# Kernel tuning notes

Hardware: AMD Instinct MI355X
Metric: run time of the kernel (lower is better)

## Reference

```python
import jax, jax.numpy as jnp
import numpy as np

B = 4096

def setup_inputs() -> dict:
    key = jax.random.key(0)
    k1, k2, k3, k4, k5 = jax.random.split(key, 5)
    x = jax.random.normal(k1, (B, 3, 32, 32), dtype=jnp.float32)
    conv_w = jax.random.normal(k2, (45, 1, 5, 5), dtype=jnp.float32) * 0.2   # grouped conv: 3 groups x 15 filters, 1 in-ch each
    conv_b = jax.random.normal(k3, (45,), dtype=jnp.float32) * 0.1
    tree_w = jax.random.normal(k4, (1, 16, 15, 3, 7, 7, 2, 2), dtype=jnp.float32) * 0.05
    tree_b = jax.random.normal(k5, (1, 16, 3, 7), dtype=jnp.float32) * 0.1
    return {"x": x, "conv_w": conv_w, "conv_b": conv_b, "tree_w": tree_w, "tree_b": tree_b}

def _forward(x, conv_w, conv_b, tree_w, tree_b):
    # grouped conv: (B,3,32,32) -> (B,45,28,28), groups=3 (channel order is group-major)
    y = jax.lax.conv_general_dilated(
        x, conv_w, window_strides=(1, 1), padding='VALID',
        dimension_numbers=('NCHW', 'OIHW', 'NCHW'), feature_group_count=3)
    y = jax.nn.sigmoid(y + conv_b[None, :, None, None])
    # max_pool2d(2): (B,45,28,28) -> (B,45,14,14)
    y = jax.lax.reduce_window(y, -jnp.inf, jax.lax.max,
                              window_dimensions=(1, 1, 2, 2),
                              window_strides=(1, 1, 2, 2), padding='VALID')
    b = y.shape[0]
    # unfold(2,2,stride=2) + reshape/transpose chain == rearrange to
    # (b, f=15, g=3, ph=7, pw=7, ki=2, kj=2); channels c = g*15 + f, H = 2*ph+ki, W = 2*pw+kj
    y = y.reshape(b, 3, 15, 7, 2, 7, 2)            # (b, g, f, ph, ki, pw, kj)
    y = y.transpose(0, 2, 1, 3, 5, 4, 6)           # (b, f, g, ph, pw, ki, kj)
    # TreeLayer: broadcast multiply with W[1,16,15,3,7,7,2,2], sum over dims (15,7,2,2)
    w = tree_w[0]                                   # (o=16, f, g, ph, pw, ki, kj)
    out = jnp.einsum('bfghwij,ofghwij->bogh', y, w)  # (b,16,3,7)
    out = jax.nn.sigmoid(out + tree_b)              # bias (1,16,3,7) broadcasts
    return out.reshape(b, -1)                       # (b, 336)

def reference(x, conv_w, conv_b, tree_w, tree_b):
    return _forward(x, conv_w, conv_b, tree_w, tree_b)
```

## Files before the change

kernel.cpp:

```cpp
#include <hip/hip_runtime.h>
#include <hip/hip_fp16.h>
#include <math.h>


#define NTW   (21 * 15 * 16 * 32)
#define TWBYTES (NTW * 2)
#define WFRAG_HALFS (3 * 2 * 64 * 8)
#define WFRAG_BYTES (WFRAG_HALFS * 2)
#define POOL_STRIDE 10240
#define POOL_BYTES (POOL_STRIDE * 2)

typedef __fp16 h2v __attribute__((ext_vector_type(2)));
typedef short short8v __attribute__((ext_vector_type(8)));
typedef float float4v __attribute__((ext_vector_type(4)));
union HU { unsigned u; h2v v; };
union FRAG { uint4 u; short8v s; };

#if defined(__has_builtin)
#if __has_builtin(__builtin_amdgcn_fdot2)
#define HAVE_FDOT2 1
#endif
#endif

__device__ __forceinline__ float sigmoidf_(float v) {
    return 1.0f / (1.0f + __expf(-v));
}
__device__ __forceinline__ h2v as_h2(unsigned x) { HU t; t.u = x; return t.v; }
__device__ __forceinline__ ushort f2bf(float v) {
    unsigned u = __float_as_uint(v);
    u += 0x7fffu + ((u >> 16) & 1u);
    return (ushort)(u >> 16);
}
__device__ __forceinline__ unsigned cvtpk_bf16(float a, float b) {
    unsigned r;
    asm volatile("v_cvt_pk_bf16_f32 %0, %1, %2" : "=v"(r) : "v"(a), "v"(b));
    return r;
}
__device__ __forceinline__ unsigned pkrtz(float a, float b) {
    HU t; t.v = __builtin_amdgcn_cvt_pkrtz(a, b); return t.u;
}

__global__ __launch_bounds__(256) void prep_all(
    const float* __restrict__ tw, const float* __restrict__ cw,
    __half* __restrict__ tw2, ushort* __restrict__ wfrag)
{
    int i = blockIdx.x * 256 + threadIdx.x;
    if (i < NTW) {
        const int e   = i & 31;
        const int o   = (i >> 5) & 15;
        const int fgh = i >> 9;
        const int f   = fgh % 15, gh = fgh / 15;
        const int g   = gh / 7,  h  = gh % 7;
        const int parity = e >> 4, rem = e & 15, half = rem >> 3, pxl = rem & 7;
        float v = 0.f;
        if (pxl < 7) {
            const int px = half * 7 + pxl;
            const int w = px >> 1, j = px & 1;
            v = tw[o * 8820 + f * 588 + g * 196 + h * 28 + w * 4 + parity * 2 + j];
        }
        tw2[i] = __float2half(v);
        return;
    }
    const int j5 = i - NTW;
    if (j5 >= 384) return;
    const int g  = j5 >> 7, rem = j5 & 127, fr = rem >> 6, l = rem & 63;
    const int f  = l & 15, q = l >> 4;
    ushort o[8];
    #pragma unroll
    for (int j = 0; j < 8; ++j) {
        float v = 0.f;
        if (f < 15 && j < 5) {
            if (fr == 0)           v = cw[(g * 15 + f) * 25 + q * 5 + j];
            else if (q == 0)       v = cw[(g * 15 + f) * 25 + 20 + j];
        }
        o[j] = f2bf(v);
    }
    ushort* d = wfrag + ((g * 2 + fr) * 64 + l) * 8;
    *(uint4*)d = make_uint4(
        (unsigned)o[0] | ((unsigned)o[1] << 16),
        (unsigned)o[2] | ((unsigned)o[3] << 16),
        (unsigned)o[4] | ((unsigned)o[5] << 16),
        (unsigned)o[6] | ((unsigned)o[7] << 16));
}

__global__ __launch_bounds__(256) void conv_pool_mfma(
    const float* __restrict__ x,
    const float* __restrict__ cb,
    const ushort* __restrict__ wfrag,
    __half* __restrict__ pool16,
    int B)
{
    __shared__ __align__(16) float  s_xf[32 * 40];
    __shared__ __align__(16) ushort s_W[32 * 30 * 8];
    __shared__ __align__(16) ushort s_pool[105 * 40];
    __shared__ float s_cb[45];
    __shared__ __align__(16) ushort s_zero[8];

    const int b = blockIdx.x;
    if (b >= B) return;
    const int t = threadIdx.x;
    const int lane = t & 63, wv = t >> 6;
    const int q = lane >> 4, oxl = lane & 15;

    if (t < 45) s_cb[t] = cb[t];
    if (t == 45) *(uint4*)&s_zero[0] = make_uint4(0u, 0u, 0u, 0u);

    float4 xpre[3];
    {
        const float4* x4 = (const float4*)(x + (size_t)b * 3072);
        #pragma unroll
        for (int g = 0; g < 3; ++g) xpre[g] = x4[g * 256 + t];
    }
    FRAG w1[3], w2[3];
    {
        const uint4* wf4 = (const uint4*)wfrag;
        #pragma unroll
        for (int g2 = 0; g2 < 3; ++g2) {
            w1[g2].u = wf4[(g2 * 2 + 0) * 64 + lane];
            w2[g2].u = wf4[(g2 * 2 + 1) * 64 + lane];
        }
    }

    const float4v z4 = {0.f, 0.f, 0.f, 0.f};
    const int row_s = t >> 3, q_s = t & 7;

    #pragma unroll 1
    for (int g = 0; g < 3; ++g) {
        *(float4*)&s_xf[row_s * 40 + q_s * 4] = xpre[g];
        if (t < 64) {
            const int r2 = t >> 1, k = t & 1;
            *(float4*)&s_xf[r2 * 40 + 32 + k * 4] = make_float4(0.f, 0.f, 0.f, 0.f);
        }
        __syncthreads();

        #pragma unroll 1
        for (int task = t; task < 480; task += 256) {
            const int row = task / 15, m = task % 15;
            const float* src = &s_xf[row * 40 + 2 * m];
            float f[10];
            #pragma unroll
            for (int k = 0; k < 5; ++k)
                *(float2*)&f[2 * k] = *(const float2*)&src[2 * k];
            const unsigned e0 = cvtpk_bf16(f[0], f[1]), e1 = cvtpk_bf16(f[2], f[3]);
            const unsigned e2 = cvtpk_bf16(f[4], f[5]), e3 = cvtpk_bf16(f[6], f[7]);
            const unsigned o0 = cvtpk_bf16(f[1], f[2]), o1 = cvtpk_bf16(f[3], f[4]);
            const unsigned o2 = cvtpk_bf16(f[5], f[6]), o3 = cvtpk_bf16(f[7], f[8]);
            ushort* wb = &s_W[(row * 30 + 2 * m) * 8];
            *(uint4*)wb       = make_uint4(e0, e1, e2, e3);
            *(uint4*)(wb + 8) = make_uint4(o0, o1, o2, o3);
        }
        __syncthreads();

        #pragma unroll 1
        for (int i = 0; i < 7; ++i) {
            const int p = wv * 7 + i;
            const int py = p >> 1, half = p & 1;
            const ushort* base = &s_W[(2 * py + q) * 240 + (oxl + 14 * half) * 8];

            FRAG a10, a11, a20, a21;
            a10.u = *(const uint4*)base;
            a11.u = *(const uint4*)(base + 240);
            const ushort* p20 = (q == 0)
                ? &s_W[(2 * py + 4) * 240 + oxl * 8 + half * 112] : &s_zero[0];
            const ushort* p21 = (q == 0)
                ? &s_W[(2 * py + 5) * 240 + oxl * 8 + half * 112] : &s_zero[0];
            a20.u = *(const uint4*)p20;
            a21.u = *(const uint4*)p21;

            float4v acc0 = __builtin_amdgcn_mfma_f32_16x16x32_bf16(a20.s, w2[g].s, z4, 0, 0, 0);
            acc0 = __builtin_amdgcn_mfma_f32_16x16x32_bf16(a10.s, w1[g].s, acc0, 0, 0, 0);
            float4v acc1 = __builtin_amdgcn_mfma_f32_16x16x32_bf16(a21.s, w2[g].s, z4, 0, 0, 0);
            acc1 = __builtin_amdgcn_mfma_f32_16x16x32_bf16(a11.s, w1[g].s, acc1, 0, 0, 0);

            const int f = oxl;
            if (f < 15) {
                const float bias = s_cb[g * 15 + f];
                const float p0 = fmaxf(fmaxf(acc0[0], acc0[1]), fmaxf(acc1[0], acc1[1]));
                const float p1 = fmaxf(fmaxf(acc0[2], acc0[3]), fmaxf(acc1[2], acc1[3]));
                const float s0 = sigmoidf_(p0 + bias);
                const float s1 = (q < 3) ? sigmoidf_(p1 + bias) : 0.f;
                const int chunk = f * 7 + (py >> 1);
                const int e0i = (py & 1) * 16 + half * 8 + 2 * q;
                *(unsigned*)&s_pool[chunk * 40 + e0i] = pkrtz(s0, s1);
            }
        }
        __syncthreads();

        {
            uint4* dst4 = (uint4*)(pool16 + (size_t)b * POOL_STRIDE) + g * 420;
            for (int i = t; i < 420; i += 256) {
                const int chunk = i >> 2, k = i & 3;
                dst4[i] = *(const uint4*)&s_pool[chunk * 40 + k * 8];
            }
        }
        __syncthreads();
    }
}

__global__ __launch_bounds__(256) void tree_kernel(
    const __half* __restrict__ pool16,
    const __half* __restrict__ tw2,
    const float* __restrict__ tb,
    float* __restrict__ out,
    int B, int nblk)
{
    __shared__ float s_red[256 * 17];

    const int cpx = nblk / 8;
    const int sid = (blockIdx.x % 8) * cpx + blockIdx.x / 8;
    const int gh = sid % 21, tile = sid / 21;
    const int g = gh / 7, h = gh % 7;

    const int t  = threadIdx.x;
    const int bl = t & 63, fg = t >> 6;
    const int b  = tile * 64 + bl;
    if (b >= B) return;

    const int f0 = fg * 4;
    const int nf = (fg < 3) ? 4 : 3;

    float acc[16];
    #pragma unroll
    for (int o = 0; o < 16; ++o) acc[o] = 0.f;

    #pragma unroll 1
    for (int fi = 0; fi < nf; ++fi) {
        const int f = f0 + fi;
        const uint4* pc = (const uint4*)(pool16 + (size_t)b * POOL_STRIDE
                                         + ((g * 15 + f) * 7 + h) * 32);
        const uint4* wc = (const uint4*)(tw2 + (size_t)((gh * 15 + f) * 16) * 32);
        uint4 pu[4];
        #pragma unroll
        for (int k = 0; k < 4; ++k) pu[k] = pc[k];
        #pragma unroll
        for (int o = 0; o < 16; ++o) {
            #pragma unroll
            for (int k = 0; k < 4; ++k) {
                const uint4 wu = wc[o * 4 + k];
#ifdef HAVE_FDOT2
                acc[o] = __builtin_amdgcn_fdot2(as_h2(pu[k].x), as_h2(wu.x), acc[o], false);
                acc[o] = __builtin_amdgcn_fdot2(as_h2(pu[k].y), as_h2(wu.y), acc[o], false);
                acc[o] = __builtin_amdgcn_fdot2(as_h2(pu[k].z), as_h2(wu.z), acc[o], false);
                acc[o] = __builtin_amdgcn_fdot2(as_h2(pu[k].w), as_h2(wu.w), acc[o], false);
#else
                const unsigned pw[4] = {pu[k].x, pu[k].y, pu[k].z, pu[k].w};
                const unsigned ww[4] = {wu.x, wu.y, wu.z, wu.w};
                #pragma unroll
                for (int qq = 0; qq < 4; ++qq) {
                    acc[o] += __half2float(__ushort_as_half((ushort)(pw[qq] & 0xffff)))
                            * __half2float(__ushort_as_half((ushort)(ww[qq] & 0xffff)));
                    acc[o] += __half2float(__ushort_as_half((ushort)(pw[qq] >> 16)))
                            * __half2float(__ushort_as_half((ushort)(ww[qq] >> 16)));
                }
#endif
            }
        }
    }

    #pragma unroll
    for (int o = 0; o < 16; ++o) s_red[t * 17 + o] = acc[o];
    __syncthreads();

    const int og = t >> 6;
    #pragma unroll
    for (int m = 0; m < 4; ++m) {
        const int o = og * 4 + m;
        float a = s_red[(0 * 64 + bl) * 17 + o] + s_red[(1 * 64 + bl) * 17 + o]
                + s_red[(2 * 64 + bl) * 17 + o] + s_red[(3 * 64 + bl) * 17 + o];
        const int idx = o * 21 + gh;
        out[(size_t)b * 336 + idx] = sigmoidf_(a + tb[idx]);
    }
}

__global__ __launch_bounds__(256) void tree_backbone_legacy(
    const float* __restrict__ x, const float* __restrict__ cw,
    const float* __restrict__ cb, const float* __restrict__ tw,
    const float* __restrict__ tb, float* __restrict__ out, int B)
{
    __shared__ float s_x[3 * 32 * 36];
    __shared__ float s_cwl[45 * 25];
    __shared__ float s_cb[45];
    __shared__ float s_pool[45][197];

    const int b = blockIdx.x;
    if (b >= B) return;
    const int t = threadIdx.x;

    const float4* xs = (const float4*)(x + (size_t)b * 3072);
    for (int i = t; i < 768; i += 256) {
        const float4 v = xs[i];
        const int g = i >> 8, rem = i & 255, r = rem >> 3, qq = rem & 7;
        const int p = ((r & 1) << 4) + (r >> 1);
        *(float4*)&s_x[(g * 32 + p) * 36 + qq * 4] = v;
    }
    for (int i = t; i < 1125; i += 256) s_cwl[i] = cw[i];
    if (t < 45) s_cb[t] = cb[t];
    __syncthreads();

    for (int task = t; task < 1260; task += 256) {
        const int h  = (task >= 630) ? 1 : 0;
        const int tt = task - 630 * h;
        const int c  = tt / 14;
        const int py = tt - c * 14;
        const int g  = c / 15;
        float aA[14], aB[14];
        #pragma unroll
        for (int d = 0; d < 14; ++d) { aA[d] = 0.f; aB[d] = 0.f; }
        #pragma unroll
        for (int dr = 0; dr < 6; ++dr) {
            const float* rp = s_x + (g * 32 + ((dr & 1) << 4) + py + (dr >> 1)) * 36 + 12 * h;
            float f[20];
            #pragma unroll
            for (int k = 0; k < 5; ++k)
                *(float4*)&f[4 * k] = *(const float4*)&rp[4 * k];
            if (dr <= 4)
                #pragma unroll
                for (int kx = 0; kx < 5; ++kx) {
                    const float w = s_cwl[c * 25 + dr * 5 + kx];
                    #pragma unroll
                    for (int d = 0; d < 14; ++d) aA[d] += f[d + kx + 2 * h] * w;
                }
            if (dr >= 1)
                #pragma unroll
                for (int kx = 0; kx < 5; ++kx) {
                    const float w = s_cwl[c * 25 + (dr - 1) * 5 + kx];
                    #pragma unroll
                    for (int d = 0; d < 14; ++d) aB[d] += f[d + kx + 2 * h] * w;
                }
        }
        float* dst = &s_pool[c][py * 14 + 7 * h];
        #pragma unroll
        for (int p = 0; p < 7; ++p) {
            float m = fmaxf(fmaxf(aA[2 * p], aA[2 * p + 1]),
                            fmaxf(aB[2 * p], aB[2 * p + 1]));
            dst[p] = sigmoidf_(m + s_cb[c]);
        }
    }
    __syncthreads();

    for (int idx = t; idx < 336; idx += 256) {
        const int o  = idx / 21;
        const int r2 = idx - o * 21;
        const int g  = r2 / 7;
        const int hh = r2 - g * 7;
        const float* wp = tw + o * 8820 + g * 196 + hh * 28;
        float acc = 0.0f;
        #pragma unroll 1
        for (int f = 0; f < 15; ++f) {
            const float4* wf = (const float4*)(wp + f * 588);
            const float* p0 = &s_pool[g * 15 + f][(2 * hh) * 14];
            const float* p1 = p0 + 14;
            #pragma unroll
            for (int w = 0; w < 7; ++w) {
                const float4 qv = wf[w];
                acc += p0[2 * w] * qv.x + p0[2 * w + 1] * qv.y
                     + p1[2 * w] * qv.z + p1[2 * w + 1] * qv.w;
            }
        }
        out[(size_t)b * 336 + idx] = sigmoidf_(acc + tb[idx]);
    }
}

extern "C" void kernel_launch(void* const* d_in, const int* in_sizes, int n_in,
                              void* d_out, int out_size, void* d_ws, size_t ws_size,
                              hipStream_t stream) {
    const float* x  = (const float*)d_in[0];
    const float* cw = (const float*)d_in[1];
    const float* cb = (const float*)d_in[2];
    const float* tw = (const float*)d_in[3];
    const float* tb = (const float*)d_in[4];
    float* out = (float*)d_out;

    const int B = in_sizes[0] / 3072;
    const size_t need = (size_t)TWBYTES + (size_t)WFRAG_BYTES + (size_t)B * POOL_BYTES;
    if (ws_size >= need) {
        __half* tw2    = (__half*)d_ws;
        ushort* wfrag  = (ushort*)((char*)d_ws + TWBYTES);
        __half* pool16 = (__half*)((char*)d_ws + TWBYTES + WFRAG_BYTES);
        const int nblk = (B / 64) * 21;
        prep_all<<<(NTW + 384 + 255) / 256, 256, 0, stream>>>(tw, cw, tw2, wfrag);
        conv_pool_mfma<<<B, 256, 0, stream>>>(x, cb, wfrag, pool16, B);
        tree_kernel<<<nblk, 256, 0, stream>>>(pool16, tw2, tb, out, B, nblk);
    } else {
        tree_backbone_legacy<<<B, 256, 0, stream>>>(x, cw, cb, tw, tb, out, B);
    }
}
```

Before: 136.3 us.

## Fuse tree layer into conv-pool kernel, keeping pooled activations in LDS

Merges the conv/pool kernel and the tree kernel into one per-sample kernel. The pooled fp16 activations for all three groups now stay in shared memory instead of going through a global buffer of about 20 KB per sample. Tree weights are re-laid out so each thread owns one (channel, row) chunk and reads coalesced weight vectors; the 16 outputs are reduced over f through shared memory in two halves. In exchange, each block re-reads the ~320 KB weight table, which must come from L2, uses more LDS, and leaves the tree dot products with uneven thread utilisation (315 chunks over 256 threads).

```diff
diff --git a/kernel.cpp b/kernel.cpp
--- a/kernel.cpp
+++ b/kernel.cpp
@@ -3,12 +3,9 @@
 #include <math.h>
 
 
-#define NTW   (21 * 15 * 16 * 32)
-#define TWBYTES (NTW * 2)
-#define WFRAG_HALFS (3 * 2 * 64 * 8)
-#define WFRAG_BYTES (WFRAG_HALFS * 2)
-#define POOL_STRIDE 10240
-#define POOL_BYTES (POOL_STRIDE * 2)
+#define NTWQ  (315 * 64)
+#define TWBYTES (NTWQ * 16)
+#define WFRAG_BYTES (3 * 2 * 64 * 8 * 2)
 
 typedef __fp16 h2v __attribute__((ext_vector_type(2)));
 typedef short short8v __attribute__((ext_vector_type(8)));
@@ -39,29 +36,50 @@
 __device__ __forceinline__ unsigned pkrtz(float a, float b) {
     HU t; t.v = __builtin_amdgcn_cvt_pkrtz(a, b); return t.u;
 }
+__device__ __forceinline__ float dot2_(unsigned p, unsigned w, float acc) {
+#ifdef HAVE_FDOT2
+    return __builtin_amdgcn_fdot2(as_h2(p), as_h2(w), acc, false);
+#else
+    acc += __half2float(__ushort_as_half((ushort)(p & 0xffff)))
+         * __half2float(__ushort_as_half((ushort)(w & 0xffff)));
+    acc += __half2float(__ushort_as_half((ushort)(p >> 16)))
+         * __half2float(__ushort_as_half((ushort)(w >> 16)));
+    return acc;
+#endif
+}
+
+__device__ __forceinline__ float tw_sigma(const float* tw, int o, int f,
+                                          int g, int h, int e) {
+    const int parity = e >> 4, rem = e & 15, half = rem >> 3, pxl = rem & 7;
+    if (pxl >= 7) return 0.f;
+    const int px = half * 7 + pxl;
+    return tw[o * 8820 + f * 588 + g * 196 + h * 28 + (px >> 1) * 4
+              + parity * 2 + (px & 1)];
+}
 
 __global__ __launch_bounds__(256) void prep_all(
     const float* __restrict__ tw, const float* __restrict__ cw,
-    __half* __restrict__ tw2, ushort* __restrict__ wfrag)
+    uint4* __restrict__ tw2t, ushort* __restrict__ wfrag)
 {
     int i = blockIdx.x * 256 + threadIdx.x;
-    if (i < NTW) {
-        const int e   = i & 31;
-        const int o   = (i >> 5) & 15;
-        const int fgh = i >> 9;
-        const int f   = fgh % 15, gh = fgh / 15;
-        const int g   = gh / 7,  h  = gh % 7;
-        const int parity = e >> 4, rem = e & 15, half = rem >> 3, pxl = rem & 7;
-        float v = 0.f;
-        if (pxl < 7) {
-            const int px = half * 7 + pxl;
-            const int w = px >> 1, j = px & 1;
-            v = tw[o * 8820 + f * 588 + g * 196 + h * 28 + w * 4 + parity * 2 + j];
-        }
-        tw2[i] = __float2half(v);
+    if (i < NTWQ) {
+        const int t2 = i % 315, ok_ = i / 315;
+        const int o = ok_ >> 2, k = ok_ & 3;
+        const int c = t2 / 7, h = t2 % 7;
+        const int g = c / 15, f = c % 15;
+        unsigned wd[4];
+        #pragma unroll
+        for (int j = 0; j < 4; ++j) {
+            const int w = k * 4 + j;
+            const float v0 = tw_sigma(tw, o, f, g, h, 2 * w);
+            const float v1 = tw_sigma(tw, o, f, g, h, 2 * w + 1);
+            wd[j] = (unsigned)__half_as_ushort(__float2half(v0))
+                  | ((unsigned)__half_as_ushort(__float2half(v1)) << 16);
+        }
+        tw2t[(size_t)ok_ * 315 + t2] = make_uint4(wd[0], wd[1], wd[2], wd[3]);
         return;
     }
-    const int j5 = i - NTW;
+    const int j5 = i - NTWQ;
     if (j5 >= 384) return;
     const int g  = j5 >> 7, rem = j5 & 127, fr = rem >> 6, l = rem & 63;
     const int f  = l & 15, q = l >> 4;
@@ -83,18 +101,22 @@
         (unsigned)o[6] | ((unsigned)o[7] << 16));
 }
 
-__global__ __launch_bounds__(256) void conv_pool_mfma(
+__global__ __launch_bounds__(256) void backbone_fused(
     const float* __restrict__ x,
     const float* __restrict__ cb,
     const ushort* __restrict__ wfrag,
-    __half* __restrict__ pool16,
+    const uint4* __restrict__ tw2t,
+    const float* __restrict__ tb,
+    float* __restrict__ out,
     int B)
 {
-    __shared__ __align__(16) float  s_xf[32 * 40];
-    __shared__ __align__(16) ushort s_W[32 * 30 * 8];
-    __shared__ __align__(16) ushort s_pool[105 * 40];
+    __shared__ __align__(16) char s_mix[20480];
+    __shared__ __align__(16) ushort s_pool[315 * 40];
     __shared__ float s_cb[45];
     __shared__ __align__(16) ushort s_zero[8];
+    float*  s_xf  = (float*)s_mix;
+    ushort* s_W   = (ushort*)(s_mix + 5120);
+    float*  s_red = (float*)s_mix;
 
     const int b = blockIdx.x;
     if (b >= B) return;
@@ -179,95 +201,93 @@
                 const float p1 = fmaxf(fmaxf(acc0[2], acc0[3]), fmaxf(acc1[2], acc1[3]));
                 const float s0 = sigmoidf_(p0 + bias);
                 const float s1 = (q < 3) ? sigmoidf_(p1 + bias) : 0.f;
-                const int chunk = f * 7 + (py >> 1);
+                const int chunk = (g * 15 + f) * 7 + (py >> 1);
                 const int e0i = (py & 1) * 16 + half * 8 + 2 * q;
                 *(unsigned*)&s_pool[chunk * 40 + e0i] = pkrtz(s0, s1);
             }
         }
         __syncthreads();
-
-        {
-            uint4* dst4 = (uint4*)(pool16 + (size_t)b * POOL_STRIDE) + g * 420;
-            for (int i = t; i < 420; i += 256) {
-                const int chunk = i >> 2, k = i & 3;
-                dst4[i] = *(const uint4*)&s_pool[chunk * 40 + k * 8];
-            }
-        }
-        __syncthreads();
-    }
-}
-
-__global__ __launch_bounds__(256) void tree_kernel(
-    const __half* __restrict__ pool16,
-    const __half* __restrict__ tw2,
-    const float* __restrict__ tb,
-    float* __restrict__ out,
-    int B, int nblk)
-{
-    __shared__ float s_red[256 * 17];
-
-    const int cpx = nblk / 8;
-    const int sid = (blockIdx.x % 8) * cpx + blockIdx.x / 8;
-    const int gh = sid % 21, tile = sid / 21;
-    const int g = gh / 7, h = gh % 7;
-
-    const int t  = threadIdx.x;
-    const int bl = t & 63, fg = t >> 6;
-    const int b  = tile * 64 + bl;
-    if (b >= B) return;
-
-    const int f0 = fg * 4;
-    const int nf = (fg < 3) ? 4 : 3;
-
-    float acc[16];
+    }
+
+    float accA[16], accB[16];
     #pragma unroll
-    for (int o = 0; o < 16; ++o) acc[o] = 0.f;
-
-    #pragma unroll 1
-    for (int fi = 0; fi < nf; ++fi) {
-        const int f = f0 + fi;
-        const uint4* pc = (const uint4*)(pool16 + (size_t)b * POOL_STRIDE
-                                         + ((g * 15 + f) * 7 + h) * 32);
-        const uint4* wc = (const uint4*)(tw2 + (size_t)((gh * 15 + f) * 16) * 32);
-        uint4 pu[4];
-        #pragma unroll
-        for (int k = 0; k < 4; ++k) pu[k] = pc[k];
+    for (int o = 0; o < 16; ++o) { accA[o] = 0.f; accB[o] = 0.f; }
+
+    if (t < 315) {
+        uint4 pk[4];
+        #pragma unroll
+        for (int k = 0; k < 4; ++k) pk[k] = *(const uint4*)&s_pool[t * 40 + k * 8];
         #pragma unroll
         for (int o = 0; o < 16; ++o) {
+            float a = 0.f;
             #pragma unroll
             for (int k = 0; k < 4; ++k) {
-                const uint4 wu = wc[o * 4 + k];
-#ifdef HAVE_FDOT2
-                acc[o] = __builtin_amdgcn_fdot2(as_h2(pu[k].x), as_h2(wu.x), acc[o], false);
-                acc[o] = __builtin_amdgcn_fdot2(as_h2(pu[k].y), as_h2(wu.y), acc[o], false);
-                acc[o] = __builtin_amdgcn_fdot2(as_h2(pu[k].z), as_h2(wu.z), acc[o], false);
-                acc[o] = __builtin_amdgcn_fdot2(as_h2(pu[k].w), as_h2(wu.w), acc[o], false);
-#else
-                const unsigned pw[4] = {pu[k].x, pu[k].y, pu[k].z, pu[k].w};
-                const unsigned ww[4] = {wu.x, wu.y, wu.z, wu.w};
-                #pragma unroll
-                for (int qq = 0; qq < 4; ++qq) {
-                    acc[o] += __half2float(__ushort_as_half((ushort)(pw[qq] & 0xffff)))
-                            * __half2float(__ushort_as_half((ushort)(ww[qq] & 0xffff)));
-                    acc[o] += __half2float(__ushort_as_half((ushort)(pw[qq] >> 16)))
-                            * __half2float(__ushort_as_half((ushort)(ww[qq] >> 16)));
-                }
-#endif
+                const uint4 wu = tw2t[(size_t)(o * 4 + k) * 315 + t];
+                a = dot2_(pk[k].x, wu.x, a);
+                a = dot2_(pk[k].y, wu.y, a);
+                a = dot2_(pk[k].z, wu.z, a);
+                a = dot2_(pk[k].w, wu.w, a);
             }
-        }
-    }
-
-    #pragma unroll
-    for (int o = 0; o < 16; ++o) s_red[t * 17 + o] = acc[o];
-    __syncthreads();
-
-    const int og = t >> 6;
-    #pragma unroll
-    for (int m = 0; m < 4; ++m) {
-        const int o = og * 4 + m;
-        float a = s_red[(0 * 64 + bl) * 17 + o] + s_red[(1 * 64 + bl) * 17 + o]
-                + s_red[(2 * 64 + bl) * 17 + o] + s_red[(3 * 64 + bl) * 17 + o];
-        const int idx = o * 21 + gh;
+            accA[o] = a;
+        }
+    }
+    if (t < 59) {
+        const int t2 = t + 256;
+        uint4 pk[4];
+        #pragma unroll
+        for (int k = 0; k < 4; ++k) pk[k] = *(const uint4*)&s_pool[t2 * 40 + k * 8];
+        #pragma unroll
+        for (int o = 0; o < 16; ++o) {
+            float a = 0.f;
+            #pragma unroll
+            for (int k = 0; k < 4; ++k) {
+                const uint4 wu = tw2t[(size_t)(o * 4 + k) * 315 + t2];
+                a = dot2_(pk[k].x, wu.x, a);
+                a = dot2_(pk[k].y, wu.y, a);
+                a = dot2_(pk[k].z, wu.z, a);
+                a = dot2_(pk[k].w, wu.w, a);
+            }
+            accB[o] = a;
+        }
+    }
+    __syncthreads();
+
+    if (t < 315) {
+        #pragma unroll
+        for (int o = 0; o < 8; ++o) s_red[t * 9 + o] = accA[o];
+    }
+    if (t < 59) {
+        #pragma unroll
+        for (int o = 0; o < 8; ++o) s_red[(t + 256) * 9 + o] = accB[o];
+    }
+    __syncthreads();
+    if (t < 168) {
+        const int o = t / 21, gh = t % 21;
+        const int g = gh / 7, h = gh % 7;
+        float a = 0.f;
+        #pragma unroll
+        for (int f = 0; f < 15; ++f)
+            a += s_red[((g * 15 + f) * 7 + h) * 9 + o];
+        out[(size_t)b * 336 + t] = sigmoidf_(a + tb[t]);
+    }
+    __syncthreads();
+    if (t < 315) {
+        #pragma unroll
+        for (int o = 8; o < 16; ++o) s_red[t * 9 + (o - 8)] = accA[o];
+    }
+    if (t < 59) {
+        #pragma unroll
+        for (int o = 8; o < 16; ++o) s_red[(t + 256) * 9 + (o - 8)] = accB[o];
+    }
+    __syncthreads();
+    if (t < 168) {
+        const int idx = 168 + t;
+        const int o = idx / 21, gh = idx % 21;
+        const int g = gh / 7, h = gh % 7;
+        float a = 0.f;
+        #pragma unroll
+        for (int f = 0; f < 15; ++f)
+            a += s_red[((g * 15 + f) * 7 + h) * 9 + (o - 8)];
         out[(size_t)b * 336 + idx] = sigmoidf_(a + tb[idx]);
     }
 }
@@ -372,15 +392,12 @@
     float* out = (float*)d_out;
 
     const int B = in_sizes[0] / 3072;
-    const size_t need = (size_t)TWBYTES + (size_t)WFRAG_BYTES + (size_t)B * POOL_BYTES;
+    const size_t need = (size_t)TWBYTES + (size_t)WFRAG_BYTES;
     if (ws_size >= need) {
-        __half* tw2    = (__half*)d_ws;
-        ushort* wfrag  = (ushort*)((char*)d_ws + TWBYTES);
-        __half* pool16 = (__half*)((char*)d_ws + TWBYTES + WFRAG_BYTES);
-        const int nblk = (B / 64) * 21;
-        prep_all<<<(NTW + 384 + 255) / 256, 256, 0, stream>>>(tw, cw, tw2, wfrag);
-        conv_pool_mfma<<<B, 256, 0, stream>>>(x, cb, wfrag, pool16, B);
-        tree_kernel<<<nblk, 256, 0, stream>>>(pool16, tw2, tb, out, B, nblk);
+        uint4*  tw2t  = (uint4*)d_ws;
+        ushort* wfrag = (ushort*)((char*)d_ws + TWBYTES);
+        prep_all<<<(NTWQ + 384 + 255) / 256, 256, 0, stream>>>(tw, cw, tw2t, wfrag);
+        backbone_fused<<<B, 256, 0, stream>>>(x, cb, wfrag, tw2t, tb, out, B);
     } else {
         tree_backbone_legacy<<<B, 256, 0, stream>>>(x, cw, cb, tw, tb, out, B);
     }
```

Measured after the change: 153.2 us. +12.4%, slower.
